# Kernel optimization log

Measured on AMD Instinct MI355X. Metric: run time of the kernel, lower is better.

Reference implementation:

```python
import jax, jax.numpy as jnp
import numpy as np

INPUT_DIM = 512
HIDDEN_DIM = 1024
NUM_LAYERS = 2
B, S = 32, 512


def _xavier(key, shape):
    fan_out, fan_in = shape
    limit = float(np.sqrt(6.0 / (fan_in + fan_out)))
    return jax.random.uniform(key, shape, jnp.float32, -limit, limit)


def setup_inputs() -> dict:
    key = jax.random.key(0)
    ks = jax.random.split(key, 8)
    x = jax.random.normal(ks[0], (B, S, INPUT_DIM), jnp.float32)
    # layer 0: input_dim -> hidden, layer 1: hidden -> hidden
    Wih0 = _xavier(ks[1], (3 * HIDDEN_DIM, INPUT_DIM))
    Whh0 = _xavier(ks[2], (3 * HIDDEN_DIM, HIDDEN_DIM))
    b0 = jnp.zeros((3 * HIDDEN_DIM,), jnp.float32)
    Wih1 = _xavier(ks[3], (3 * HIDDEN_DIM, HIDDEN_DIM))
    Whh1 = _xavier(ks[4], (3 * HIDDEN_DIM, HIDDEN_DIM))
    b1 = jnp.zeros((3 * HIDDEN_DIM,), jnp.float32)
    Wlin = _xavier(ks[5], (INPUT_DIM, HIDDEN_DIM))
    blin = jnp.zeros((INPUT_DIM,), jnp.float32)
    return {"x": x, "Wih0": Wih0, "Whh0": Whh0, "b0": b0,
            "Wih1": Wih1, "Whh1": Whh1, "b1": b1,
            "Wlin": Wlin, "blin": blin}


def _gru_layer(x_tm, h0, Wih, Whh, b):
    # x_tm: [S, B, D_in] time-major; h0: [B, H]
    H = HIDDEN_DIM
    Whn = Whh[2 * H: 3 * H]  # [H, H] used twice per the original cell

    def step(h, x_t):
        gates = x_t @ Wih.T + h @ Whh.T + b          # [B, 3H]
        r, z, n = jnp.split(gates, 3, axis=1)
        r = jax.nn.sigmoid(r)
        z = jax.nn.sigmoid(z)
        # NOTE: original cell adds h@Whn a second time, scaled by r (nonstandard)
        n = jnp.tanh(n + r * (h @ Whn.T))
        h_new = (1.0 - z) * n + z * h
        return h_new, h_new

    h_last, ys = jax.lax.scan(step, h0, x_tm)
    return ys, h_last  # ys: [S, B, H]


def reference(x, Wih0, Whh0, b0, Wih1, Whh1, b1, Wlin, blin):
    # dropout=0.0 -> identity (eval mode)
    x_tm = jnp.swapaxes(x, 0, 1)  # [S, B, D]
    h0 = jnp.zeros((x.shape[0], HIDDEN_DIM), x.dtype)
    y0, h_last0 = _gru_layer(x_tm, h0, Wih0, Whh0, b0)
    y1, h_last1 = _gru_layer(y0, h0, Wih1, Whh1, b1)
    layer_output = jnp.swapaxes(y1, 0, 1)            # [B, S, H]
    out = layer_output @ Wlin.T + blin               # [B, S, INPUT_DIM]
    new_hidden = jnp.stack([h_last0, h_last1], axis=0)  # [L, B, H]
    return out, new_hidden
```

## Files before the change

kernel.cpp:

```cpp
#include <hip/hip_runtime.h>
#include <math.h>

#define B_  32
#define S_  512
#define H_  1024
#define G3_ 3072
#define SENT32 0x7F7F7F7Fu

typedef __attribute__((ext_vector_type(8))) short bf16x8;
typedef __attribute__((ext_vector_type(4))) float f32x4;
typedef __attribute__((ext_vector_type(4))) unsigned int u32x4;

__device__ __forceinline__ unsigned short f2bf(float f) {
  unsigned int u = __float_as_uint(f);
  u = (u + 0x7FFFu + ((u >> 16) & 1u)) >> 16;
  return (unsigned short)u;
}

__device__ __forceinline__ void ld4_mall(const unsigned short* p, u32x4& r) {
  asm volatile("global_load_dwordx4 %0, %1, off sc0 sc1" : "=v"(r) : "v"(p));
}
__device__ __forceinline__ void st_mall_b32(unsigned short* p, unsigned int v) {
  asm volatile("global_store_dword %0, %1, off sc0 sc1" :: "v"(p), "v"(v) : "memory");
}

#define BAR_LGKM() do {                                   \
  __builtin_amdgcn_sched_barrier(0);                      \
  asm volatile("s_waitcnt lgkmcnt(0)" ::: "memory");      \
  __builtin_amdgcn_s_barrier();                           \
  __builtin_amdgcn_sched_barrier(0);                      \
} while (0)

__global__ void cast_f32_bf16(const float* __restrict__ in, unsigned short* __restrict__ out, int n) {
  int i = blockIdx.x * 256 + threadIdx.x;
  if (i < n) out[i] = f2bf(in[i]);
}

__global__ void cast_transpose_x(const float* __restrict__ x, unsigned short* __restrict__ xtm) {
  int s = blockIdx.x & 511, b = blockIdx.x >> 9;
  int k = threadIdx.x * 4;
  float4 v = *(const float4*)(x + ((size_t)b * S_ + s) * 512 + k);
  ushort4 o = { f2bf(v.x), f2bf(v.y), f2bf(v.z), f2bf(v.w) };
  *(ushort4*)(xtm + ((size_t)s * B_ + b) * 512 + k) = o;
}


__global__ __launch_bounds__(512, 2)
void gru_fused(const unsigned short* __restrict__ wih0, const unsigned short* __restrict__ whh0,
               const float* __restrict__ b0,
               const unsigned short* __restrict__ wih1, const unsigned short* __restrict__ whh1,
               const float* __restrict__ b1,
               const unsigned short* __restrict__ xtm, const unsigned short* __restrict__ zerosB,
               unsigned short* __restrict__ hx0, unsigned short* __restrict__ hx1,
               const unsigned short* __restrict__ wlin, const float* __restrict__ blin,
               float* __restrict__ out,
               float* __restrict__ hlast0, float* __restrict__ hlast1) {
  __shared__ __align__(16) float part[8 * 2 * 3 * 64 * 4];
  const int tid  = threadIdx.x;
  const int lane = tid & 63;
  const int w    = tid >> 6;
  const int r16  = lane & 15;
  const int q    = lane >> 4;

  union AU { unsigned int dd[4]; u32x4 u4; bf16x8 v; };

  if (blockIdx.x >= 128) {
    const int nj0 = ((int)blockIdx.x - 128) * 16;
    const int kbase = w * 128;
    const int blkbase = kbase >> 4;
    bf16x8 bwp[4];
#pragma unroll
    for (int c = 0; c < 4; ++c)
      bwp[c] = *(const bf16x8*)(wlin + (size_t)(nj0 + r16) * H_ + kbase + c * 32 + q * 8);
    const int eb = tid >> 4, ejj = tid & 15;
    const int em = eb >> 4, eq2 = (eb >> 2) & 3, ereg = eb & 3;
    const float bl = blin[nj0 + ejj];
    const int hxLaneOff = ((q >> 1) * 512) + r16 * 16 + (q & 1) * 8;

    for (int t = 0; t < S_; ++t) {
      const unsigned short* hp = hx1 + ((size_t)t * 64 + blkbase) * 512 + hxLaneOff;
      AU a0[4], a1[4];
      int spins = 0;
      for (;;) {
#pragma unroll
        for (int c = 0; c < 4; ++c) {
          ld4_mall(hp + c * 1024, a0[c].u4);
          ld4_mall(hp + c * 1024 + 256, a1[c].u4);
        }
        asm volatile("s_waitcnt vmcnt(0)"
          : "+v"(a0[0].u4), "+v"(a0[1].u4), "+v"(a0[2].u4), "+v"(a0[3].u4),
            "+v"(a1[0].u4), "+v"(a1[1].u4), "+v"(a1[2].u4), "+v"(a1[3].u4)
          :: "memory");
        __builtin_amdgcn_sched_barrier(0);
        int ok = 1;
#pragma unroll
        for (int c = 0; c < 4; ++c)
#pragma unroll
          for (int d = 0; d < 4; ++d)
            ok &= (a0[c].dd[d] != SENT32) & (a1[c].dd[d] != SENT32);
        if (__all(ok)) break;
        if (++spins > (1 << 21)) break;
        if (spins > 8) __builtin_amdgcn_s_sleep(1);
      }

      f32x4 acc[2];
#pragma unroll
      for (int m = 0; m < 2; ++m)
#pragma unroll
        for (int u = 0; u < 4; ++u) acc[m][u] = 0.f;
#pragma unroll
      for (int c = 0; c < 4; ++c) {
        acc[0] = __builtin_amdgcn_mfma_f32_16x16x32_bf16(a0[c].v, bwp[c], acc[0], 0, 0, 0);
        acc[1] = __builtin_amdgcn_mfma_f32_16x16x32_bf16(a1[c].v, bwp[c], acc[1], 0, 0, 0);
      }
#pragma unroll
      for (int m = 0; m < 2; ++m)
        *(f32x4*)&part[((w * 2 + m) * 64 + lane) * 4] = acc[m];
      BAR_LGKM();
      {
        float s = 0.f;
#pragma unroll
        for (int ww = 0; ww < 8; ++ww)
          s += part[((ww * 2 + em) * 64 + eq2 * 16 + ejj) * 4 + ereg];
        out[((size_t)eb * S_ + t) * 512 + nj0 + ejj] = s + bl;
      }
      BAR_LGKM();
    }
    return;
  }

  const bool L1  = blockIdx.x >= 64;
  const int  j0  = (L1 ? (int)blockIdx.x - 64 : (int)blockIdx.x) * 16;
  const int  myblk = j0 >> 4;
  const bool hiw = w >= 4;

  const unsigned short* Wsrc;
  int wstride, kbase, ncha;
  if (!L1) {
    if (!hiw) { Wsrc = wih0; wstride = 512;  kbase = w * 128;       ncha = 4; }
    else      { Wsrc = whh0; wstride = 1024; kbase = (w - 4) * 256; ncha = 8; }
  } else {
    if (!hiw) { Wsrc = wih1; wstride = 1024; kbase = w * 256;       ncha = 8; }
    else      { Wsrc = whh1; wstride = 1024; kbase = (w - 4) * 256; ncha = 8; }
  }
  const int blkbase = kbase >> 4;

  bf16x8 bw[3][8];
#pragma unroll
  for (int g = 0; g < 3; ++g)
#pragma unroll
    for (int c = 0; c < 8; ++c)
      if (c < ncha)
        bw[g][c] = *(const bf16x8*)(Wsrc + (size_t)(g * H_ + j0 + r16) * wstride + kbase + c * 32 + q * 8);

  const int eb  = tid >> 4;
  const int ejj = tid & 15;
  const int em  = eb >> 4, eq2 = (eb >> 2) & 3, ereg = eb & 3;
  const float* bias = L1 ? b1 : b0;
  const float brv = bias[j0 + ejj];
  const float bzv = bias[H_ + j0 + ejj];
  const float bnv = bias[2 * H_ + j0 + ejj];
  float phv = 0.f;

  unsigned short* hxbuf = L1 ? hx1 : hx0;
  float*          hlast = L1 ? hlast1 : hlast0;

  const int hxLaneOff = ((q >> 1) * 512) + r16 * 16 + (q & 1) * 8;

  for (int t = 0; t < S_; ++t) {
    AU a0[8], a1[8];
    bool plain;
    const unsigned short* pp = nullptr;
    int pstride = 0;
    const unsigned short* hp = nullptr;
    if (!hiw) {
      if (!L1) { plain = true;  pp = xtm + (size_t)t * B_ * 512; pstride = 512; }
      else     { plain = false; hp = hx0 + ((size_t)t * 64 + blkbase) * 512 + hxLaneOff; }
    } else {
      if (t == 0) { plain = true;  pp = zerosB; pstride = 1024; }
      else        { plain = false; hp = hxbuf + ((size_t)(t - 1) * 64 + blkbase) * 512 + hxLaneOff; }
    }
    if (plain) {
      const unsigned short* ap0 = pp + (size_t)r16 * pstride + kbase + q * 8;
      const unsigned short* ap1 = ap0 + 16 * pstride;
#pragma unroll
      for (int c = 0; c < 8; ++c) if (c < ncha) {
        a0[c].v = *(const bf16x8*)(ap0 + c * 32);
        a1[c].v = *(const bf16x8*)(ap1 + c * 32);
      }
    } else {
      int spins = 0;
      for (;;) {
#pragma unroll
        for (int c = 0; c < 8; ++c) {
          ld4_mall(hp + c * 1024, a0[c].u4);
          ld4_mall(hp + c * 1024 + 256, a1[c].u4);
        }
        asm volatile("s_waitcnt vmcnt(0)"
          : "+v"(a0[0].u4), "+v"(a0[1].u4), "+v"(a0[2].u4), "+v"(a0[3].u4),
            "+v"(a0[4].u4), "+v"(a0[5].u4), "+v"(a0[6].u4), "+v"(a0[7].u4),
            "+v"(a1[0].u4), "+v"(a1[1].u4), "+v"(a1[2].u4), "+v"(a1[3].u4),
            "+v"(a1[4].u4), "+v"(a1[5].u4), "+v"(a1[6].u4), "+v"(a1[7].u4)
          :: "memory");
        __builtin_amdgcn_sched_barrier(0);
        int ok = 1;
#pragma unroll
        for (int c = 0; c < 8; ++c)
#pragma unroll
          for (int d = 0; d < 4; ++d)
            ok &= (a0[c].dd[d] != SENT32) & (a1[c].dd[d] != SENT32);
        if (__all(ok)) break;
        if (++spins > (1 << 20)) break;
        if (spins > 8) __builtin_amdgcn_s_sleep(1);
      }
    }

    f32x4 acc[2][3];
#pragma unroll
    for (int m = 0; m < 2; ++m)
#pragma unroll
      for (int g = 0; g < 3; ++g)
#pragma unroll
        for (int u = 0; u < 4; ++u) acc[m][g][u] = 0.f;

#pragma unroll
    for (int c = 0; c < 8; ++c) if (c < ncha)
#pragma unroll
      for (int g = 0; g < 3; ++g) {
        acc[0][g] = __builtin_amdgcn_mfma_f32_16x16x32_bf16(a0[c].v, bw[g][c], acc[0][g], 0, 0, 0);
        acc[1][g] = __builtin_amdgcn_mfma_f32_16x16x32_bf16(a1[c].v, bw[g][c], acc[1][g], 0, 0, 0);
      }

#pragma unroll
    for (int m = 0; m < 2; ++m)
#pragma unroll
      for (int g = 0; g < 3; ++g)
        *(f32x4*)&part[(((w * 2 + m) * 3 + g) * 64 + lane) * 4] = acc[m][g];
    BAR_LGKM();

    {
      float hr = 0.f, hz = 0.f, nx = 0.f, nh = 0.f;
#pragma unroll
      for (int ww = 0; ww < 8; ++ww) {
        int base = (ww * 2 + em) * 3;
        float vr = part[((base + 0) * 64 + eq2 * 16 + ejj) * 4 + ereg];
        float vz = part[((base + 1) * 64 + eq2 * 16 + ejj) * 4 + ereg];
        float vn = part[((base + 2) * 64 + eq2 * 16 + ejj) * 4 + ereg];
        hr += vr; hz += vz;
        if (ww < 4) nx += vn; else nh += vn;
      }
      float r  = __builtin_amdgcn_rcpf(1.f + __expf(-(hr + brv)));
      float z  = __builtin_amdgcn_rcpf(1.f + __expf(-(hz + bzv)));
      float a2 = nx + bnv + nh + r * nh;
      float nn = 1.f - 2.f * __builtin_amdgcn_rcpf(__expf(2.f * a2) + 1.f);
      float hv = (1.f - z) * nn + z * phv;
      phv = hv;
      float other = __shfl_xor(hv, 1);
      if ((ejj & 1) == 0) {
        unsigned int pk = (unsigned int)f2bf(hv) | ((unsigned int)f2bf(other) << 16);
        st_mall_b32(hxbuf + ((size_t)t * 64 + myblk) * 512 + eb * 16 + ejj, pk);
        if (t == S_ - 1) {
          hlast[eb * H_ + j0 + ejj]     = hv;
          hlast[eb * H_ + j0 + ejj + 1] = other;
        }
      }
    }
    BAR_LGKM();
  }
}

extern "C" void kernel_launch(void* const* d_in, const int* in_sizes, int n_in,
                              void* d_out, int out_size, void* d_ws, size_t ws_size,
                              hipStream_t stream) {
  const float* x    = (const float*)d_in[0];
  const float* Wih0 = (const float*)d_in[1];
  const float* Whh0 = (const float*)d_in[2];
  const float* b0   = (const float*)d_in[3];
  const float* Wih1 = (const float*)d_in[4];
  const float* Whh1 = (const float*)d_in[5];
  const float* b1   = (const float*)d_in[6];
  const float* Wlin = (const float*)d_in[7];
  const float* blin = (const float*)d_in[8];
  float* out = (float*)d_out;

  char* p = (char*)d_ws;
  size_t off = 0;
  auto alloc = [&](size_t bytes) { void* r = p + off; off += (bytes + 255) & ~(size_t)255; return r; };

  unsigned short* xtm   = (unsigned short*)alloc((size_t)8388608 * 2);
  unsigned short* wih0b = (unsigned short*)alloc((size_t)1572864 * 2);
  unsigned short* whh0b = (unsigned short*)alloc((size_t)3145728 * 2);
  unsigned short* wih1b = (unsigned short*)alloc((size_t)3145728 * 2);
  unsigned short* whh1b = (unsigned short*)alloc((size_t)3145728 * 2);
  unsigned short* wlinb = (unsigned short*)alloc((size_t)524288 * 2);
  unsigned short* hx0   = (unsigned short*)alloc((size_t)16777216 * 2);
  unsigned short* hx1   = (unsigned short*)alloc((size_t)16777216 * 2);
  unsigned short* zerosB= (unsigned short*)alloc((size_t)B_ * H_ * 2);

  (void)hipMemsetAsync(hx0, 0x7F, (size_t)16777216 * 2, stream);
  (void)hipMemsetAsync(hx1, 0x7F, (size_t)16777216 * 2, stream);
  (void)hipMemsetAsync(zerosB, 0, (size_t)B_ * H_ * 2, stream);

  auto cast = [&](const float* in, unsigned short* o, int n) {
    cast_f32_bf16<<<n / 256, 256, 0, stream>>>(in, o, n);
  };
  cast_transpose_x<<<16384, 128, 0, stream>>>(x, xtm);
  cast(Wih0, wih0b, 1572864);
  cast(Whh0, whh0b, 3145728);
  cast(Wih1, wih1b, 3145728);
  cast(Whh1, whh1b, 3145728);
  cast(Wlin, wlinb, 524288);

  float* hlast0 = out + 8388608;
  float* hlast1 = out + 8388608 + B_ * H_;

  gru_fused<<<160, 512, 0, stream>>>(wih0b, whh0b, b0, wih1b, whh1b, b1,
                                     xtm, zerosB, hx0, hx1, wlinb, blin, out,
                                     hlast0, hlast1);
}
```

Before: 1.942 ms.

## Fuse fp32-to-bf16 casts into persistent GRU kernel and drop prep launches

```diff
diff --git a/kernel.cpp b/kernel.cpp
--- a/kernel.cpp
+++ b/kernel.cpp
@@ -4,7 +4,6 @@
 #define B_  32
 #define S_  512
 #define H_  1024
-#define G3_ 3072
 #define SENT32 0x7F7F7F7Fu
 
 typedef __attribute__((ext_vector_type(8))) short bf16x8;
@@ -31,28 +30,24 @@
   __builtin_amdgcn_sched_barrier(0);                      \
 } while (0)
 
-__global__ void cast_f32_bf16(const float* __restrict__ in, unsigned short* __restrict__ out, int n) {
-  int i = blockIdx.x * 256 + threadIdx.x;
-  if (i < n) out[i] = f2bf(in[i]);
-}
-
-__global__ void cast_transpose_x(const float* __restrict__ x, unsigned short* __restrict__ xtm) {
-  int s = blockIdx.x & 511, b = blockIdx.x >> 9;
-  int k = threadIdx.x * 4;
-  float4 v = *(const float4*)(x + ((size_t)b * S_ + s) * 512 + k);
-  ushort4 o = { f2bf(v.x), f2bf(v.y), f2bf(v.z), f2bf(v.w) };
-  *(ushort4*)(xtm + ((size_t)s * B_ + b) * 512 + k) = o;
+__device__ __forceinline__ bf16x8 ld8_f32_to_bf16(const float* p) {
+  float4 a = *(const float4*)p;
+  float4 b = *(const float4*)(p + 4);
+  union { unsigned short s[8]; bf16x8 v; } u;
+  u.s[0] = f2bf(a.x); u.s[1] = f2bf(a.y); u.s[2] = f2bf(a.z); u.s[3] = f2bf(a.w);
+  u.s[4] = f2bf(b.x); u.s[5] = f2bf(b.y); u.s[6] = f2bf(b.z); u.s[7] = f2bf(b.w);
+  return u.v;
 }
 
 
 __global__ __launch_bounds__(512, 2)
-void gru_fused(const unsigned short* __restrict__ wih0, const unsigned short* __restrict__ whh0,
+void gru_fused(const float* __restrict__ x,
+               const float* __restrict__ wih0, const float* __restrict__ whh0,
                const float* __restrict__ b0,
-               const unsigned short* __restrict__ wih1, const unsigned short* __restrict__ whh1,
+               const float* __restrict__ wih1, const float* __restrict__ whh1,
                const float* __restrict__ b1,
-               const unsigned short* __restrict__ xtm, const unsigned short* __restrict__ zerosB,
+               const float* __restrict__ wlin, const float* __restrict__ blin,
                unsigned short* __restrict__ hx0, unsigned short* __restrict__ hx1,
-               const unsigned short* __restrict__ wlin, const float* __restrict__ blin,
                float* __restrict__ out,
                float* __restrict__ hlast0, float* __restrict__ hlast1) {
   __shared__ __align__(16) float part[8 * 2 * 3 * 64 * 4];
@@ -71,7 +66,7 @@
     bf16x8 bwp[4];
 #pragma unroll
     for (int c = 0; c < 4; ++c)
-      bwp[c] = *(const bf16x8*)(wlin + (size_t)(nj0 + r16) * H_ + kbase + c * 32 + q * 8);
+      bwp[c] = ld8_f32_to_bf16(wlin + (size_t)(nj0 + r16) * H_ + kbase + c * 32 + q * 8);
     const int eb = tid >> 4, ejj = tid & 15;
     const int em = eb >> 4, eq2 = (eb >> 2) & 3, ereg = eb & 3;
     const float bl = blin[nj0 + ejj];
@@ -99,8 +94,8 @@
           for (int d = 0; d < 4; ++d)
             ok &= (a0[c].dd[d] != SENT32) & (a1[c].dd[d] != SENT32);
         if (__all(ok)) break;
-        if (++spins > (1 << 21)) break;
-        if (spins > 8) __builtin_amdgcn_s_sleep(1);
+        if (++spins > (1 << 16)) break;
+        __builtin_amdgcn_s_sleep(32);
       }
 
       f32x4 acc[2];
@@ -134,7 +129,7 @@
   const int  myblk = j0 >> 4;
   const bool hiw = w >= 4;
 
-  const unsigned short* Wsrc;
+  const float* Wsrc;
   int wstride, kbase, ncha;
   if (!L1) {
     if (!hiw) { Wsrc = wih0; wstride = 512;  kbase = w * 128;       ncha = 4; }
@@ -151,7 +146,7 @@
 #pragma unroll
     for (int c = 0; c < 8; ++c)
       if (c < ncha)
-        bw[g][c] = *(const bf16x8*)(Wsrc + (size_t)(g * H_ + j0 + r16) * wstride + kbase + c * 32 + q * 8);
+        bw[g][c] = ld8_f32_to_bf16(Wsrc + (size_t)(g * H_ + j0 + r16) * wstride + kbase + c * 32 + q * 8);
 
   const int eb  = tid >> 4;
   const int ejj = tid & 15;
@@ -169,26 +164,23 @@
 
   for (int t = 0; t < S_; ++t) {
     AU a0[8], a1[8];
-    bool plain;
-    const unsigned short* pp = nullptr;
-    int pstride = 0;
-    const unsigned short* hp = nullptr;
-    if (!hiw) {
-      if (!L1) { plain = true;  pp = xtm + (size_t)t * B_ * 512; pstride = 512; }
-      else     { plain = false; hp = hx0 + ((size_t)t * 64 + blkbase) * 512 + hxLaneOff; }
+    if (!hiw && !L1) {
+      const float* xr0 = x + ((size_t)r16 * S_ + t) * 512 + kbase + q * 8;
+      const float* xr1 = x + ((size_t)(r16 + 16) * S_ + t) * 512 + kbase + q * 8;
+#pragma unroll
+      for (int c = 0; c < 8; ++c) if (c < ncha) {
+        a0[c].v = ld8_f32_to_bf16(xr0 + c * 32);
+        a1[c].v = ld8_f32_to_bf16(xr1 + c * 32);
+      }
+    } else if (hiw && t == 0) {
+#pragma unroll
+      for (int c = 0; c < 8; ++c)
+#pragma unroll
+        for (int d = 0; d < 4; ++d) { a0[c].dd[d] = 0u; a1[c].dd[d] = 0u; }
     } else {
-      if (t == 0) { plain = true;  pp = zerosB; pstride = 1024; }
-      else        { plain = false; hp = hxbuf + ((size_t)(t - 1) * 64 + blkbase) * 512 + hxLaneOff; }
-    }
-    if (plain) {
-      const unsigned short* ap0 = pp + (size_t)r16 * pstride + kbase + q * 8;
-      const unsigned short* ap1 = ap0 + 16 * pstride;
-#pragma unroll
-      for (int c = 0; c < 8; ++c) if (c < ncha) {
-        a0[c].v = *(const bf16x8*)(ap0 + c * 32);
-        a1[c].v = *(const bf16x8*)(ap1 + c * 32);
-      }
-    } else {
+      const unsigned short* hp = (!hiw)
+        ? hx0   + ((size_t)t * 64 + blkbase) * 512 + hxLaneOff
+        : hxbuf + ((size_t)(t - 1) * 64 + blkbase) * 512 + hxLaneOff;
       int spins = 0;
       for (;;) {
 #pragma unroll
@@ -287,34 +279,15 @@
   size_t off = 0;
   auto alloc = [&](size_t bytes) { void* r = p + off; off += (bytes + 255) & ~(size_t)255; return r; };
 
-  unsigned short* xtm   = (unsigned short*)alloc((size_t)8388608 * 2);
-  unsigned short* wih0b = (unsigned short*)alloc((size_t)1572864 * 2);
-  unsigned short* whh0b = (unsigned short*)alloc((size_t)3145728 * 2);
-  unsigned short* wih1b = (unsigned short*)alloc((size_t)3145728 * 2);
-  unsigned short* whh1b = (unsigned short*)alloc((size_t)3145728 * 2);
-  unsigned short* wlinb = (unsigned short*)alloc((size_t)524288 * 2);
-  unsigned short* hx0   = (unsigned short*)alloc((size_t)16777216 * 2);
-  unsigned short* hx1   = (unsigned short*)alloc((size_t)16777216 * 2);
-  unsigned short* zerosB= (unsigned short*)alloc((size_t)B_ * H_ * 2);
+  unsigned short* hx0 = (unsigned short*)alloc((size_t)16777216 * 2);
+  unsigned short* hx1 = (unsigned short*)alloc((size_t)16777216 * 2);
 
   (void)hipMemsetAsync(hx0, 0x7F, (size_t)16777216 * 2, stream);
   (void)hipMemsetAsync(hx1, 0x7F, (size_t)16777216 * 2, stream);
-  (void)hipMemsetAsync(zerosB, 0, (size_t)B_ * H_ * 2, stream);
-
-  auto cast = [&](const float* in, unsigned short* o, int n) {
-    cast_f32_bf16<<<n / 256, 256, 0, stream>>>(in, o, n);
-  };
-  cast_transpose_x<<<16384, 128, 0, stream>>>(x, xtm);
-  cast(Wih0, wih0b, 1572864);
-  cast(Whh0, whh0b, 3145728);
-  cast(Wih1, wih1b, 3145728);
-  cast(Whh1, whh1b, 3145728);
-  cast(Wlin, wlinb, 524288);
 
   float* hlast0 = out + 8388608;
   float* hlast1 = out + 8388608 + B_ * H_;
 
-  gru_fused<<<160, 512, 0, stream>>>(wih0b, whh0b, b0, wih1b, whh1b, b1,
-                                     xtm, zerosB, hx0, hx1, wlinb, blin, out,
-                                     hlast0, hlast1);
-}
+  gru_fused<<<160, 512, 0, stream>>>(x, Wih0, Whh0, b0, Wih1, Whh1, b1,
+                                     Wlin, blin, hx0, hx1, out, hlast0, hlast1);
+}
```

After: 2.309 ms. +18.9%, slower.
